# Optimization experiments

Measured on AMD Instinct MI355X. Metric: run time of the kernel, lower is better.

## Reference

```python
import jax, jax.numpy as jnp
import numpy as np

N_FFT = 1024
N_STAGES = 4
BATCH = 16384


def _mod_seq(order):
    mset = [0]
    for o in range(order):
        step = 2 ** o
        mset = [v for x in mset for v in (x, x + step)]
    return mset


def _partial_bit_reversal(N, order):
    m = np.zeros((N, N), dtype=np.float32)
    base = 2 ** order
    k = 0
    for p in _mod_seq(order):
        for j in range(N // base):
            m[j * base + p, k] = 1.0
            k += 1
    return m


def setup_inputs() -> dict:
    key = jax.random.key(0)
    x = jax.random.normal(key, (BATCH, N_FFT), dtype=jnp.float32)
    n_sub = N_FFT // 2 ** N_STAGES  # 64: dense sub-DFT size
    dft = np.fft.fft(np.eye(n_sub))
    inp = {
        "x": x,
        "perm": jnp.asarray(_partial_bit_reversal(N_FFT, N_STAGES)),
        "fft_real": jnp.asarray(dft.real, dtype=jnp.float32),
        "fft_imag": jnp.asarray(dft.imag, dtype=jnp.float32),
    }
    stage = N_FFT // 2 ** (N_STAGES - 1)  # 128, doubles each stage
    for s in range(N_STAGES):
        w = np.exp(-2j * np.pi / stage) ** np.arange(stage // 2)
        inp[f"tw_real_{s}"] = jnp.asarray(w.real, dtype=jnp.float32)
        inp[f"tw_imag_{s}"] = jnp.asarray(w.imag, dtype=jnp.float32)
        stage *= 2
    return inp


def _fft_forward(x, perm, fft_real, fft_imag, tws):
    # bit-reversal permutation (matmul against 0/1 matrix, as in the original)
    y = x @ perm
    n_chunks = 2 ** N_STAGES
    # stack chunks: (n_chunks, B, n_sub)
    c = jnp.stack(jnp.split(y, n_chunks, axis=-1), axis=0)
    ev, od = c[0::2], c[1::2]  # (m, B, s) each, m = n_chunks // 2
    # dense sub-DFTs (x @ M.T)
    ev_r = jnp.einsum('mbs,ts->mbt', ev, fft_real)
    ev_i = jnp.einsum('mbs,ts->mbt', ev, fft_imag)
    od_r = jnp.einsum('mbs,ts->mbt', od, fft_real)
    od_i = jnp.einsum('mbs,ts->mbt', od, fft_imag)
    # butterfly twiddle stages; m halves and s doubles each stage
    for tr, ti in tws:
        todd_r = tr * od_r - ti * od_i
        todd_i = tr * od_i + ti * od_r
        real = jnp.concatenate([ev_r + todd_r, ev_r - todd_r], axis=-1)
        imag = jnp.concatenate([ev_i + todd_i, ev_i - todd_i], axis=-1)
        ev_r, od_r = real[0::2], real[1::2]
        ev_i, od_i = imag[0::2], imag[1::2]
    return ev_r[0], ev_i[0]


def reference(x, perm, fft_real, fft_imag,
              tw_real_0, tw_imag_0, tw_real_1, tw_imag_1,
              tw_real_2, tw_imag_2, tw_real_3, tw_imag_3):
    tws = [(tw_real_0, tw_imag_0), (tw_real_1, tw_imag_1),
           (tw_real_2, tw_imag_2), (tw_real_3, tw_imag_3)]
    return _fft_forward(x, perm, fft_real, fft_imag, tws)
```

## Files before the change

kernel.cpp:

```cpp
#include <hip/hip_runtime.h>


#define N_FFT 1024
#define BATCH 16384
#define TPB   256

typedef float f4 __attribute__((ext_vector_type(4)));

__device__ __forceinline__ int pad16(int a) { return a + (a >> 4); }

__device__ __forceinline__ float2 cmul(float2 a, float2 b) {
    return make_float2(a.x * b.x - a.y * b.y, a.x * b.y + a.y * b.x);
}
__device__ __forceinline__ float2 cadd(float2 a, float2 b) { return make_float2(a.x + b.x, a.y + b.y); }
__device__ __forceinline__ float2 csub(float2 a, float2 b) { return make_float2(a.x - b.x, a.y - b.y); }

#define LDS_FENCE() do { asm volatile("s_waitcnt lgkmcnt(0)" ::: "memory"); \
                         __builtin_amdgcn_sched_barrier(0); } while (0)

__device__ __forceinline__ void bf4(float2& A, float2& B, float2& C, float2& D, float2 w1)
{
    float2 t0 = cadd(A, C), t1 = csub(A, C);
    float2 t2 = cadd(B, D);
    float2 t3 = make_float2(B.y - D.y, D.x - B.x);
    float2 w2 = cmul(w1, w1);
    float2 w3 = cmul(w1, w2);
    A = cadd(t0, t2);
    B = cmul(cadd(t1, t3), w1);
    C = cmul(csub(t0, t2), w2);
    D = cmul(csub(t1, t3), w3);
}
__device__ __forceinline__ void bf4_nw(float2& A, float2& B, float2& C, float2& D)
{
    float2 t0 = cadd(A, C), t1 = csub(A, C);
    float2 t2 = cadd(B, D);
    float2 t3 = make_float2(B.y - D.y, D.x - B.x);
    A = cadd(t0, t2);
    B = cadd(t1, t3);
    C = csub(t0, t2);
    D = csub(t1, t3);
}

__global__ __launch_bounds__(TPB, 4) void fft1024_kernel(
    const float* __restrict__ x,
    const float* __restrict__ twr,
    const float* __restrict__ twi,
    float* __restrict__ outr,
    float* __restrict__ outi)
{
    __shared__ __align__(16) float2 exbuf[4][1088];
    __shared__ __align__(16) float2 tws[256];

    const int tid = threadIdx.x;
    const int T   = tid & 63;
    const int wv  = tid >> 6;
    float2* __restrict__ ex = exbuf[wv];

    if (tid < 64) {
        f4 re = reinterpret_cast<const f4*>(twr)[tid];
        f4 im = reinterpret_cast<const f4*>(twi)[tid];
        #pragma unroll
        for (int j = 0; j < 4; ++j)
            tws[4 * tid + j] = make_float2(re[j], im[j]);
    }

    const long long r0 = 8LL * blockIdx.x + 2 * wv;

    {
        const f4* __restrict__ xv = reinterpret_cast<const f4*>(x + r0 * N_FFT);
        f4* xs4 = reinterpret_cast<f4*>(ex);
        #pragma unroll
        for (int s = 0; s < 8; ++s)
            xs4[T + 64 * s] = xv[T + 64 * s];
    }
    __syncthreads();

    float2 z[16];
    {
        const float* xs = reinterpret_cast<const float*>(ex);
        #pragma unroll
        for (int q = 0; q < 16; ++q)
            z[q] = make_float2(xs[T + 64 * q], xs[1024 + T + 64 * q]);
    }
    LDS_FENCE();

    #pragma unroll
    for (int u = 0; u < 4; ++u)
        bf4(z[u], z[u + 4], z[u + 8], z[u + 12], tws[T + 64 * u]);
    {
        float2 wA = tws[4 * T];
        #pragma unroll
        for (int r = 0; r < 4; ++r) {
            bf4(z[4 * r], z[4 * r + 1], z[4 * r + 2], z[4 * r + 3], wA);
            ex[pad16(16 * T + r)]      = z[4 * r];
            ex[pad16(16 * T + 4 + r)]  = z[4 * r + 1];
            ex[pad16(16 * T + 8 + r)]  = z[4 * r + 2];
            ex[pad16(16 * T + 12 + r)] = z[4 * r + 3];
        }
    }
    __syncthreads();

    #pragma unroll
    for (int q = 0; q < 16; ++q)
        z[q] = ex[pad16(T + 64 * q)];
    LDS_FENCE();

    #pragma unroll
    for (int u = 0; u < 4; ++u)
        bf4(z[u], z[u + 4], z[u + 8], z[u + 12], tws[(T + 64 * u) & ~15]);
    {
        float2 wB = tws[(T >> 4) << 6];
        const int base2 = ((T >> 4) << 8) + (T & 15);
        #pragma unroll
        for (int p = 0; p < 4; ++p) {
            bf4(z[4 * p], z[4 * p + 1], z[4 * p + 2], z[4 * p + 3], wB);
            ex[pad16(base2 + 16 * p)]       = z[4 * p];
            ex[pad16(base2 + 16 * p + 64)]  = z[4 * p + 1];
            ex[pad16(base2 + 16 * p + 128)] = z[4 * p + 2];
            ex[pad16(base2 + 16 * p + 192)] = z[4 * p + 3];
        }
    }
    __syncthreads();

    #pragma unroll
    for (int q = 0; q < 16; ++q)
        z[q] = ex[pad16(T + 64 * q)];
    #pragma unroll
    for (int u = 0; u < 4; ++u) {
        bf4_nw(z[u], z[u + 4], z[u + 8], z[u + 12]);
        ex[pad16(T + 64 * u)]       = z[u];
        ex[pad16(T + 64 * u + 256)] = z[u + 4];
        ex[pad16(T + 64 * u + 512)] = z[u + 8];
        ex[pad16(T + 64 * u + 768)] = z[u + 12];
    }
    __syncthreads();

    f4* or0v = reinterpret_cast<f4*>(outr + r0 * N_FFT);
    f4* oi0v = reinterpret_cast<f4*>(outi + r0 * N_FFT);
    #pragma unroll
    for (int g = 0; g < 4; ++g) {
        const int k0 = 256 * g + 4 * T;
        const int pk = pad16(k0);
        f4 vr0, vi0, vr1, vi1;
        #pragma unroll
        for (int e = 0; e < 4; ++e) {
            const int k  = k0 + e;
            const int nk = (N_FFT - k) & (N_FFT - 1);
            float2 zk = ex[pk + e];
            float2 zn = ex[pad16(nk)];
            vr0[e] = 0.5f * (zk.x + zn.x);
            vi0[e] = 0.5f * (zk.y - zn.y);
            vr1[e] = 0.5f * (zk.y + zn.y);
            vi1[e] = 0.5f * (zn.x - zk.x);
        }
        __builtin_nontemporal_store(vr0, or0v + 64 * g + T);
        __builtin_nontemporal_store(vi0, oi0v + 64 * g + T);
        __builtin_nontemporal_store(vr1, or0v + 256 + 64 * g + T);
        __builtin_nontemporal_store(vi1, oi0v + 256 + 64 * g + T);
    }
}

extern "C" void kernel_launch(void* const* d_in, const int* in_sizes, int n_in,
                              void* d_out, int out_size, void* d_ws, size_t ws_size,
                              hipStream_t stream) {
    const float* x   = (const float*)d_in[0];
    const float* twr = (const float*)d_in[10];
    const float* twi = (const float*)d_in[11];
    float* outr = (float*)d_out;
    float* outi = outr + (size_t)BATCH * N_FFT;
    fft1024_kernel<<<BATCH / 8, TPB, 0, stream>>>(x, twr, twi, outr, outi);
}
```

Baseline: 207.1 us.

## Process two row pairs per wave with direct global loads and wave-local syncs

```diff
diff --git a/kernel.cpp b/kernel.cpp
--- a/kernel.cpp
+++ b/kernel.cpp
@@ -41,6 +41,88 @@
     D = csub(t1, t3);
 }
 
+__device__ __forceinline__ void fft_pair(float2* __restrict__ z,
+                                         float2* __restrict__ ex,
+                                         const float2* __restrict__ tws,
+                                         int T,
+                                         f4* __restrict__ or0v,
+                                         f4* __restrict__ oi0v)
+{
+    #pragma unroll
+    for (int u = 0; u < 4; ++u)
+        bf4(z[u], z[u + 4], z[u + 8], z[u + 12], tws[T + 64 * u]);
+    {
+        float2 wA = tws[4 * T];
+        #pragma unroll
+        for (int r = 0; r < 4; ++r) {
+            bf4(z[4 * r], z[4 * r + 1], z[4 * r + 2], z[4 * r + 3], wA);
+            ex[pad16(16 * T + r)]      = z[4 * r];
+            ex[pad16(16 * T + 4 + r)]  = z[4 * r + 1];
+            ex[pad16(16 * T + 8 + r)]  = z[4 * r + 2];
+            ex[pad16(16 * T + 12 + r)] = z[4 * r + 3];
+        }
+    }
+    LDS_FENCE();
+
+    #pragma unroll
+    for (int q = 0; q < 16; ++q)
+        z[q] = ex[pad16(T + 64 * q)];
+    LDS_FENCE();
+
+    #pragma unroll
+    for (int u = 0; u < 4; ++u)
+        bf4(z[u], z[u + 4], z[u + 8], z[u + 12], tws[(T + 64 * u) & ~15]);
+    {
+        float2 wB = tws[(T >> 4) << 6];
+        const int base2 = ((T >> 4) << 8) + (T & 15);
+        #pragma unroll
+        for (int p = 0; p < 4; ++p) {
+            bf4(z[4 * p], z[4 * p + 1], z[4 * p + 2], z[4 * p + 3], wB);
+            ex[pad16(base2 + 16 * p)]       = z[4 * p];
+            ex[pad16(base2 + 16 * p + 64)]  = z[4 * p + 1];
+            ex[pad16(base2 + 16 * p + 128)] = z[4 * p + 2];
+            ex[pad16(base2 + 16 * p + 192)] = z[4 * p + 3];
+        }
+    }
+    LDS_FENCE();
+
+    #pragma unroll
+    for (int q = 0; q < 16; ++q)
+        z[q] = ex[pad16(T + 64 * q)];
+    #pragma unroll
+    for (int u = 0; u < 4; ++u) {
+        bf4_nw(z[u], z[u + 4], z[u + 8], z[u + 12]);
+        ex[pad16(T + 64 * u)]       = z[u];
+        ex[pad16(T + 64 * u + 256)] = z[u + 4];
+        ex[pad16(T + 64 * u + 512)] = z[u + 8];
+        ex[pad16(T + 64 * u + 768)] = z[u + 12];
+    }
+    LDS_FENCE();
+
+    #pragma unroll
+    for (int g = 0; g < 4; ++g) {
+        const int k0 = 256 * g + 4 * T;
+        const int pk = pad16(k0);
+        f4 vr0, vi0, vr1, vi1;
+        #pragma unroll
+        for (int e = 0; e < 4; ++e) {
+            const int k  = k0 + e;
+            const int nk = (N_FFT - k) & (N_FFT - 1);
+            float2 zk = ex[pk + e];
+            float2 zn = ex[pad16(nk)];
+            vr0[e] = 0.5f * (zk.x + zn.x);
+            vi0[e] = 0.5f * (zk.y - zn.y);
+            vr1[e] = 0.5f * (zk.y + zn.y);
+            vi1[e] = 0.5f * (zn.x - zk.x);
+        }
+        __builtin_nontemporal_store(vr0, or0v + 64 * g + T);
+        __builtin_nontemporal_store(vi0, oi0v + 64 * g + T);
+        __builtin_nontemporal_store(vr1, or0v + 256 + 64 * g + T);
+        __builtin_nontemporal_store(vi1, oi0v + 256 + 64 * g + T);
+    }
+    LDS_FENCE();
+}
+
 __global__ __launch_bounds__(TPB, 4) void fft1024_kernel(
     const float* __restrict__ x,
     const float* __restrict__ twr,
@@ -64,100 +146,33 @@
             tws[4 * tid + j] = make_float2(re[j], im[j]);
     }
 
-    const long long r0 = 8LL * blockIdx.x + 2 * wv;
+    const long long rowA = 16LL * blockIdx.x + 4 * wv;
+    const long long rowB = rowA + 2;
 
+    float2 zA[16];
     {
-        const f4* __restrict__ xv = reinterpret_cast<const f4*>(x + r0 * N_FFT);
-        f4* xs4 = reinterpret_cast<f4*>(ex);
+        const float* __restrict__ xa = x + rowA * N_FFT;
         #pragma unroll
-        for (int s = 0; s < 8; ++s)
-            xs4[T + 64 * s] = xv[T + 64 * s];
+        for (int q = 0; q < 16; ++q)
+            zA[q] = make_float2(xa[T + 64 * q], xa[N_FFT + T + 64 * q]);
     }
+    float2 zB[16];
+    {
+        const float* __restrict__ xb = x + rowB * N_FFT;
+        #pragma unroll
+        for (int q = 0; q < 16; ++q)
+            zB[q] = make_float2(xb[T + 64 * q], xb[N_FFT + T + 64 * q]);
+    }
+
     __syncthreads();
 
-    float2 z[16];
-    {
-        const float* xs = reinterpret_cast<const float*>(ex);
-        #pragma unroll
-        for (int q = 0; q < 16; ++q)
-            z[q] = make_float2(xs[T + 64 * q], xs[1024 + T + 64 * q]);
-    }
-    LDS_FENCE();
+    fft_pair(zA, ex, tws, T,
+             reinterpret_cast<f4*>(outr + rowA * N_FFT),
+             reinterpret_cast<f4*>(outi + rowA * N_FFT));
 
-    #pragma unroll
-    for (int u = 0; u < 4; ++u)
-        bf4(z[u], z[u + 4], z[u + 8], z[u + 12], tws[T + 64 * u]);
-    {
-        float2 wA = tws[4 * T];
-        #pragma unroll
-        for (int r = 0; r < 4; ++r) {
-            bf4(z[4 * r], z[4 * r + 1], z[4 * r + 2], z[4 * r + 3], wA);
-            ex[pad16(16 * T + r)]      = z[4 * r];
-            ex[pad16(16 * T + 4 + r)]  = z[4 * r + 1];
-            ex[pad16(16 * T + 8 + r)]  = z[4 * r + 2];
-            ex[pad16(16 * T + 12 + r)] = z[4 * r + 3];
-        }
-    }
-    __syncthreads();
-
-    #pragma unroll
-    for (int q = 0; q < 16; ++q)
-        z[q] = ex[pad16(T + 64 * q)];
-    LDS_FENCE();
-
-    #pragma unroll
-    for (int u = 0; u < 4; ++u)
-        bf4(z[u], z[u + 4], z[u + 8], z[u + 12], tws[(T + 64 * u) & ~15]);
-    {
-        float2 wB = tws[(T >> 4) << 6];
-        const int base2 = ((T >> 4) << 8) + (T & 15);
-        #pragma unroll
-        for (int p = 0; p < 4; ++p) {
-            bf4(z[4 * p], z[4 * p + 1], z[4 * p + 2], z[4 * p + 3], wB);
-            ex[pad16(base2 + 16 * p)]       = z[4 * p];
-            ex[pad16(base2 + 16 * p + 64)]  = z[4 * p + 1];
-            ex[pad16(base2 + 16 * p + 128)] = z[4 * p + 2];
-            ex[pad16(base2 + 16 * p + 192)] = z[4 * p + 3];
-        }
-    }
-    __syncthreads();
-
-    #pragma unroll
-    for (int q = 0; q < 16; ++q)
-        z[q] = ex[pad16(T + 64 * q)];
-    #pragma unroll
-    for (int u = 0; u < 4; ++u) {
-        bf4_nw(z[u], z[u + 4], z[u + 8], z[u + 12]);
-        ex[pad16(T + 64 * u)]       = z[u];
-        ex[pad16(T + 64 * u + 256)] = z[u + 4];
-        ex[pad16(T + 64 * u + 512)] = z[u + 8];
-        ex[pad16(T + 64 * u + 768)] = z[u + 12];
-    }
-    __syncthreads();
-
-    f4* or0v = reinterpret_cast<f4*>(outr + r0 * N_FFT);
-    f4* oi0v = reinterpret_cast<f4*>(outi + r0 * N_FFT);
-    #pragma unroll
-    for (int g = 0; g < 4; ++g) {
-        const int k0 = 256 * g + 4 * T;
-        const int pk = pad16(k0);
-        f4 vr0, vi0, vr1, vi1;
-        #pragma unroll
-        for (int e = 0; e < 4; ++e) {
-            const int k  = k0 + e;
-            const int nk = (N_FFT - k) & (N_FFT - 1);
-            float2 zk = ex[pk + e];
-            float2 zn = ex[pad16(nk)];
-            vr0[e] = 0.5f * (zk.x + zn.x);
-            vi0[e] = 0.5f * (zk.y - zn.y);
-            vr1[e] = 0.5f * (zk.y + zn.y);
-            vi1[e] = 0.5f * (zn.x - zk.x);
-        }
-        __builtin_nontemporal_store(vr0, or0v + 64 * g + T);
-        __builtin_nontemporal_store(vi0, oi0v + 64 * g + T);
-        __builtin_nontemporal_store(vr1, or0v + 256 + 64 * g + T);
-        __builtin_nontemporal_store(vi1, oi0v + 256 + 64 * g + T);
-    }
+    fft_pair(zB, ex, tws, T,
+             reinterpret_cast<f4*>(outr + rowB * N_FFT),
+             reinterpret_cast<f4*>(outi + rowB * N_FFT));
 }
 
 extern "C" void kernel_launch(void* const* d_in, const int* in_sizes, int n_in,
@@ -168,5 +183,5 @@
     const float* twi = (const float*)d_in[11];
     float* outr = (float*)d_out;
     float* outi = outr + (size_t)BATCH * N_FFT;
-    fft1024_kernel<<<BATCH / 8, TPB, 0, stream>>>(x, twr, twi, outr, outi);
+    fft1024_kernel<<<BATCH / 16, TPB, 0, stream>>>(x, twr, twi, outr, outi);
 }
```

Result: slower. 224.3 us (+8.3%).
